# Kernel tuning notes

Hardware: AMD Instinct MI355X
Metric: run time of the kernel (lower is better)

The kernel has to match this reference:

```python
import jax, jax.numpy as jnp
import numpy as np

B, T, H, L, O = 256, 512, 512, 2, 2

def setup_inputs() -> dict:
    key = jax.random.key(0)
    ks = jax.random.split(key, 9)
    s = 0.05
    return {
        "x": jax.random.normal(ks[0], (B, T), jnp.float32),
        # input-side gate weights, layer 0 (input dim 1); gate order: [r, z, n]
        "Wi0": jax.random.normal(ks[1], (3, H, 1), jnp.float32) * s,
        "bi0": jax.random.normal(ks[2], (3, H), jnp.float32) * s,
        # input-side gate weights, layers 1..L-1 (input dim H)
        "Wi_rest": jax.random.normal(ks[3], (L - 1, 3, H, H), jnp.float32) * s,
        "bi_rest": jax.random.normal(ks[4], (L - 1, 3, H), jnp.float32) * s,
        # hidden-side gate weights for all layers
        "Wh": jax.random.normal(ks[5], (L, 3, H, H), jnp.float32) * s,
        "bh": jax.random.normal(ks[6], (L, 3, H), jnp.float32) * s,
        "fc_w": jax.random.normal(ks[7], (O, H), jnp.float32) * s,
        "fc_b": jax.random.normal(ks[8], (O,), jnp.float32) * s,
    }


def reference(x, Wi0, bi0, Wi_rest, bi_rest, Wh, bh, fc_w, fc_b):
    nL = Wh.shape[0]
    hsz = Wh.shape[-1]
    bsz = x.shape[0]

    def step(h, x_t):  # h: [L, B, H], x_t: [B]
        inp = x_t[:, None]  # [B, 1]
        new_h = []
        for l in range(nL):
            # fuse the 3 input-side and 3 hidden-side gate GEMMs into one einsum each
            if l == 0:
                gi = jnp.einsum('bi,ghi->gbh', inp, Wi0) + bi0[:, None, :]
            else:
                gi = jnp.einsum('bi,ghi->gbh', inp, Wi_rest[l - 1]) + bi_rest[l - 1, :, None, :]
            gh = jnp.einsum('bi,ghi->gbh', h[l], Wh[l]) + bh[l, :, None, :]
            r = jax.nn.sigmoid(gi[0] + gh[0])
            z = jax.nn.sigmoid(gi[1] + gh[1])
            n = jnp.tanh(gi[2] + r * gh[2])
            hl = (1.0 - z) * n + z * h[l]
            new_h.append(hl)
            inp = hl
        return jnp.stack(new_h), None

    h0 = jnp.zeros((nL, bsz, hsz), x.dtype)
    h_final, _ = jax.lax.scan(step, h0, x.T)  # scan over time axis
    return h_final[-1] @ fc_w.T + fc_b  # [B, O]
```

## Files before the change

### kernel.cpp

```cpp
#include <hip/hip_runtime.h>


#define TLEN 512
#define HDIM 512
#define MROW 32
#define NL0  8
#define WPG  24
#define GRID 192
#define U0   64
#define U1   32
#define HSZ  (MROW*HDIM)
#define ROWB 1040
#define DEPTH 4

#define RT_BAR 10000000ULL

typedef __attribute__((ext_vector_type(8))) short bf16x8;
typedef __attribute__((ext_vector_type(4))) float f32x4;

#define AT_LD64(p)   __hip_atomic_load((const unsigned long long*)(p), __ATOMIC_RELAXED, __HIP_MEMORY_SCOPE_AGENT)
#define AT_LD32(p)   __hip_atomic_load((const unsigned*)(p), __ATOMIC_RELAXED, __HIP_MEMORY_SCOPE_AGENT)
#define AT_ST16(p,v) __hip_atomic_store((unsigned short*)(p), (v), __ATOMIC_RELAXED, __HIP_MEMORY_SCOPE_AGENT)
#define AT_ST32(p,v) __hip_atomic_store((unsigned*)(p), (v), __ATOMIC_RELAXED, __HIP_MEMORY_SCOPE_AGENT)
#define AT_ST32F(p,v) __hip_atomic_store((float*)(p), (v), __ATOMIC_RELAXED, __HIP_MEMORY_SCOPE_AGENT)

__device__ __forceinline__ unsigned short f2bf(float f){
  unsigned u = __builtin_bit_cast(unsigned, f);
  u = (u + 0x7FFFu + ((u>>16)&1u)) >> 16;
  return (unsigned short)u;
}
__device__ __forceinline__ float sigm(float v){ return 1.f/(1.f + __expf(-v)); }
__device__ __forceinline__ float tanh_f(float v){ return 1.f - 2.f/(__expf(2.f*v)+1.f); }

__device__ __forceinline__ bool wait_flags(unsigned* fl, int tA, int tB, int* sab){
  if (threadIdx.x < 64){
    const int lane = threadIdx.x;
    const int tgt = (lane<8) ? tA : (lane<24 ? tB : (int)0x80000000);
    const unsigned long long t0 = __builtin_amdgcn_s_memrealtime();
    int ab = 0;
    for(;;){
      int f = (lane<24) ? (int)AT_LD32(fl + lane) : 0x7fffffff;
      if (__ballot(f >= tgt) == ~0ULL) break;
      if (__builtin_amdgcn_s_memrealtime() - t0 > RT_BAR){ ab = 1; break; }
      __builtin_amdgcn_s_sleep(1);
    }
    if (lane==0) *sab = ab;
  }
  __syncthreads();
  __builtin_amdgcn_sched_barrier(0);
  return *sab != 0;
}

__device__ __forceinline__ void stage16(const unsigned short* src, unsigned short* shDst, int tid){
  unsigned long long hb[16];
  #pragma unroll
  for (int i=0;i<16;++i)
    hb[i] = AT_LD64((const char*)src + tid*8 + i*2048);
  #pragma unroll
  for (int i=0;i<16;++i){
    int flat = tid*8 + i*2048;
    *(unsigned long long*)((char*)shDst + (flat>>10)*ROWB + (flat&1023)) = hb[i];
  }
}

extern "C" __global__ void __launch_bounds__(256,1)
gru_persistent(const float* __restrict__ x,
               const float* __restrict__ Wi0,
               const float* __restrict__ bi0,
               const float* __restrict__ Wi1,
               const float* __restrict__ bi1,
               const float* __restrict__ Wh,
               const float* __restrict__ bh,
               const float* __restrict__ fcw,
               const float* __restrict__ fcb,
               float* __restrict__ out,
               unsigned* __restrict__ flg,
               unsigned short* __restrict__ h0g,
               unsigned short* __restrict__ h1g,
               float* __restrict__ h1f)
{
  __shared__ unsigned short shA[MROW*(ROWB/2)];
  __shared__ unsigned short shB[MROW*(ROWB/2)];
  __shared__ float shG[MROW*192];
  __shared__ int s_ab;

  const int tid  = threadIdx.x;
  const int lane = tid & 63;
  const int w    = tid >> 6;
  const int grp  = blockIdx.x & 7;
  const int wgid = blockIdx.x >> 3;
  const int g32  = grp*32;

  unsigned* fl = flg + grp*64;
  unsigned short* h0 = h0g + grp*DEPTH*HSZ;
  unsigned short* h1 = h1g + grp*DEPTH*HSZ;

  if (wgid < NL0){
    const int u0   = wgid*U0;
    const int colb = w*48;

    bf16x8 bfr[3][16];
    #pragma unroll
    for (int nt=0; nt<3; ++nt){
      int col = colb + nt*16 + (lane&15);
      int g = col>>6, uu = col&63;
      const float* wrow = Wh + (size_t)(g*HDIM + u0 + uu)*HDIM;
      #pragma unroll
      for (int ks=0; ks<16; ++ks){
        int k = ks*32 + (lane>>4)*8;
        const float4 f0 = *(const float4*)(wrow + k);
        const float4 f1 = *(const float4*)(wrow + k + 4);
        bf16x8 v;
        v[0]=(short)f2bf(f0.x); v[1]=(short)f2bf(f0.y); v[2]=(short)f2bf(f0.z); v[3]=(short)f2bf(f0.w);
        v[4]=(short)f2bf(f1.x); v[5]=(short)f2bf(f1.y); v[6]=(short)f2bf(f1.z); v[7]=(short)f2bf(f1.w);
        bfr[nt][ks]=v;
      }
    }
    const int ua   = tid & 63;
    const int brow = (tid>>6)*8;
    float wi0v[3], bi0v[3], bh0v[3];
    #pragma unroll
    for (int g=0; g<3; ++g){
      wi0v[g] = Wi0[g*HDIM + u0+ua];
      bi0v[g] = bi0[g*HDIM + u0+ua];
      bh0v[g] = bh [g*HDIM + u0+ua];
    }
    float h_own[8];
    #pragma unroll
    for (int j=0;j<8;++j) h_own[j]=0.f;

    for (int s=0; s<TLEN; ++s){
      float xv[8];
      #pragma unroll
      for (int j=0;j<8;++j) xv[j] = x[(g32+brow+j)*TLEN + s];

      if (wait_flags(fl, s, s-3, &s_ab)) return;

      stage16(h0 + ((s-1)&3)*HSZ, shA, tid);
      __syncthreads();
      f32x4 acc[2][3] = {};
      #pragma unroll
      for (int ks=0; ks<16; ++ks){
        int koff = ks*64 + (lane>>4)*16;
        bf16x8 a0 = *(const bf16x8*)((const char*)shA + (lane&15)*ROWB + koff);
        bf16x8 a1 = *(const bf16x8*)((const char*)shA + ((lane&15)+16)*ROWB + koff);
        #pragma unroll
        for (int nt=0; nt<3; ++nt){
          acc[0][nt] = __builtin_amdgcn_mfma_f32_16x16x32_bf16(a0, bfr[nt][ks], acc[0][nt],0,0,0);
          acc[1][nt] = __builtin_amdgcn_mfma_f32_16x16x32_bf16(a1, bfr[nt][ks], acc[1][nt],0,0,0);
        }
      }
      #pragma unroll
      for (int mt=0; mt<2; ++mt)
        #pragma unroll
        for (int nt=0; nt<3; ++nt)
          #pragma unroll
          for (int j=0;j<4;++j){
            int b = mt*16 + (lane>>4)*4 + j;
            shG[b*192 + colb + nt*16 + (lane&15)] = acc[mt][nt][j];
          }
      __syncthreads();
      unsigned short* dstA = h0 + (s&3)*HSZ;
      #pragma unroll
      for (int j=0;j<8;++j){
        int b = brow + j;
        float G0 = shG[b*192 + ua]       + bh0v[0];
        float G1 = shG[b*192 + 64 + ua]  + bh0v[1];
        float G2 = shG[b*192 + 128 + ua] + bh0v[2];
        float r_ = sigm(fmaf(xv[j], wi0v[0], bi0v[0]) + G0);
        float z_ = sigm(fmaf(xv[j], wi0v[1], bi0v[1]) + G1);
        float n_ = tanh_f(fmaf(xv[j], wi0v[2], bi0v[2]) + r_*G2);
        float hn = (1.f - z_)*n_ + z_*h_own[j];
        h_own[j] = hn;
        AT_ST16(&dstA[b*HDIM + u0 + ua], f2bf(hn));
      }
      asm volatile("s_waitcnt vmcnt(0)" ::: "memory");
      __syncthreads();
      if (tid==0) AT_ST32(fl + wgid, (unsigned)(s+1));
    }
    if (wgid==0){
      if (wait_flags(fl, (int)0x80000000, TLEN, &s_ab)) return;
      int p = tid>>2, kl = tid&3;
      int b = p>>1, o = p&1;
      const char* h8 = (const char*)(h1f + (size_t)(g32+b)*HDIM + kl*128);
      const float2* w2 = (const float2*)(fcw + o*HDIM + kl*128);
      float a2 = 0.f;
      #pragma unroll
      for (int k=0;k<64;++k){
        unsigned long long v = AT_LD64(h8 + k*8);
        float2 hv = __builtin_bit_cast(float2, v);
        float2 wv = w2[k];
        a2 = fmaf(hv.x, wv.x, fmaf(hv.y, wv.y, a2));
      }
      a2 += __shfl_xor(a2, 1);
      a2 += __shfl_xor(a2, 2);
      if (kl==0) out[(g32+b)*2 + o] = a2 + fcb[o];
    }
  } else {
    const int u1   = (wgid-NL0)*U1;
    const int colb = (w<2) ? w*48 : 96 + (w-2)*48;

    bf16x8 bfr[3][16];
    #pragma unroll
    for (int nt=0; nt<3; ++nt){
      int col = colb + nt*16 + (lane&15);
      const float* wrow;
      if (w < 2){ int g = col>>5, uu = col&31;
        wrow = Wi1 + (size_t)(g*HDIM + u1 + uu)*HDIM;
      } else {    int c2 = col-96; int g = c2>>5, uu = c2&31;
        wrow = Wh + (size_t)((3+g)*HDIM + u1 + uu)*HDIM;
      }
      #pragma unroll
      for (int ks=0; ks<16; ++ks){
        int k = ks*32 + (lane>>4)*8;
        const float4 f0 = *(const float4*)(wrow + k);
        const float4 f1 = *(const float4*)(wrow + k + 4);
        bf16x8 v;
        v[0]=(short)f2bf(f0.x); v[1]=(short)f2bf(f0.y); v[2]=(short)f2bf(f0.z); v[3]=(short)f2bf(f0.w);
        v[4]=(short)f2bf(f1.x); v[5]=(short)f2bf(f1.y); v[6]=(short)f2bf(f1.z); v[7]=(short)f2bf(f1.w);
        bfr[nt][ks]=v;
      }
    }
    const int ua   = tid & 31;
    const int brow = (tid>>5)*4;
    float bi1v[3], bh1v[3];
    #pragma unroll
    for (int g=0; g<3; ++g){
      bi1v[g] = bi1[g*HDIM + u1+ua];
      bh1v[g] = bh [(3+g)*HDIM + u1+ua];
    }
    float h_own[4];
    #pragma unroll
    for (int j=0;j<4;++j) h_own[j]=0.f;

    for (int t=1; t<=TLEN; ++t){
      if (wait_flags(fl, t, t-1, &s_ab)) return;

      stage16(h0 + ((t-1)&3)*HSZ, shA, tid);
      stage16(h1 + ((t-2)&3)*HSZ, shB, tid);
      __syncthreads();
      const char* shSrc = (w<2) ? (const char*)shA : (const char*)shB;
      f32x4 acc[2][3] = {};
      #pragma unroll
      for (int ks=0; ks<16; ++ks){
        int koff = ks*64 + (lane>>4)*16;
        bf16x8 a0 = *(const bf16x8*)(shSrc + (lane&15)*ROWB + koff);
        bf16x8 a1 = *(const bf16x8*)(shSrc + ((lane&15)+16)*ROWB + koff);
        #pragma unroll
        for (int nt=0; nt<3; ++nt){
          acc[0][nt] = __builtin_amdgcn_mfma_f32_16x16x32_bf16(a0, bfr[nt][ks], acc[0][nt],0,0,0);
          acc[1][nt] = __builtin_amdgcn_mfma_f32_16x16x32_bf16(a1, bfr[nt][ks], acc[1][nt],0,0,0);
        }
      }
      #pragma unroll
      for (int mt=0; mt<2; ++mt)
        #pragma unroll
        for (int nt=0; nt<3; ++nt)
          #pragma unroll
          for (int j=0;j<4;++j){
            int b = mt*16 + (lane>>4)*4 + j;
            shG[b*192 + colb + nt*16 + (lane&15)] = acc[mt][nt][j];
          }
      __syncthreads();
      unsigned short* dstB = h1 + ((t-1)&3)*HSZ;
      #pragma unroll
      for (int j=0;j<4;++j){
        int b = brow + j;
        float gi0 = shG[b*192 + ua]        + bi1v[0];
        float gi1 = shG[b*192 + 32 + ua]   + bi1v[1];
        float gi2 = shG[b*192 + 64 + ua]   + bi1v[2];
        float gh0 = shG[b*192 + 96 + ua]   + bh1v[0];
        float gh1 = shG[b*192 + 128 + ua]  + bh1v[1];
        float gh2 = shG[b*192 + 160 + ua]  + bh1v[2];
        float r_ = sigm(gi0+gh0);
        float z_ = sigm(gi1+gh1);
        float n_ = tanh_f(gi2 + r_*gh2);
        float hn = (1.f - z_)*n_ + z_*h_own[j];
        h_own[j] = hn;
        AT_ST16(&dstB[b*HDIM + u1 + ua], f2bf(hn));
        if (t == TLEN) AT_ST32F(&h1f[(size_t)(g32+b)*HDIM + u1 + ua], hn);
      }
      asm volatile("s_waitcnt vmcnt(0)" ::: "memory");
      __syncthreads();
      if (tid==0) AT_ST32(fl + wgid, (unsigned)t);
    }
  }
}

extern "C" void kernel_launch(void* const* d_in, const int* in_sizes, int n_in,
                              void* d_out, int out_size, void* d_ws, size_t ws_size,
                              hipStream_t stream)
{
  const float* x   = (const float*)d_in[0];
  const float* Wi0 = (const float*)d_in[1];
  const float* bi0 = (const float*)d_in[2];
  const float* Wi1 = (const float*)d_in[3];
  const float* bi1 = (const float*)d_in[4];
  const float* Wh  = (const float*)d_in[5];
  const float* bh  = (const float*)d_in[6];
  const float* fcw = (const float*)d_in[7];
  const float* fcb = (const float*)d_in[8];
  float* out = (float*)d_out;

  unsigned*       flg = (unsigned*)d_ws;
  unsigned short* h0g = (unsigned short*)((char*)d_ws + 4096);
  unsigned short* h1g = (unsigned short*)((char*)d_ws + 4096 + 1048576);
  float*          h1f = (float*)((char*)d_ws + 4096 + 2*1048576);

  hipMemsetAsync(d_ws, 0, 4096 + 2*1048576 + 524288, stream);
  gru_persistent<<<GRID, 256, 0, stream>>>(x,Wi0,bi0,Wi1,bi1,Wh,bh,fcw,fcb,out,
                                           flg,h0g,h1g,h1f);
}
```

Before: 2.426 ms.

## Have each workgroup serve two batch groups, halving the grid to 96 blocks

Each persistent workgroup now loops over two batch groups of 32 rows per timestep instead of one, and the grid shrinks from 192 to 96 blocks. The register-resident bf16 weight fragments are reused across both groups, which halves the number of blocks that load and convert weights and that take part in flag polling. In exchange, each block runs two dependent stage/MFMA/activation/flag sequences back to back per step. That lengthens the serial critical path per timestep unless the two groups' waits overlap with each other's work.

```diff
diff --git a/kernel.cpp b/kernel.cpp
--- a/kernel.cpp
+++ b/kernel.cpp
@@ -6,7 +6,7 @@
 #define MROW 32
 #define NL0  8
 #define WPG  24
-#define GRID 192
+#define GRID 96
 #define U0   64
 #define U1   32
 #define HSZ  (MROW*HDIM)
@@ -87,13 +87,8 @@
   const int tid  = threadIdx.x;
   const int lane = tid & 63;
   const int w    = tid >> 6;
-  const int grp  = blockIdx.x & 7;
-  const int wgid = blockIdx.x >> 3;
-  const int g32  = grp*32;
-
-  unsigned* fl = flg + grp*64;
-  unsigned short* h0 = h0g + grp*DEPTH*HSZ;
-  unsigned short* h1 = h1g + grp*DEPTH*HSZ;
+  const int pair = blockIdx.x & 3;
+  const int wgid = blockIdx.x >> 2;
 
   if (wgid < NL0){
     const int u0   = wgid*U0;
@@ -125,76 +120,92 @@
       bi0v[g] = bi0[g*HDIM + u0+ua];
       bh0v[g] = bh [g*HDIM + u0+ua];
     }
-    float h_own[8];
-    #pragma unroll
-    for (int j=0;j<8;++j) h_own[j]=0.f;
+    float h_own[2][8];
+    #pragma unroll
+    for (int gi=0; gi<2; ++gi)
+      #pragma unroll
+      for (int j=0;j<8;++j) h_own[gi][j]=0.f;
 
     for (int s=0; s<TLEN; ++s){
-      float xv[8];
-      #pragma unroll
-      for (int j=0;j<8;++j) xv[j] = x[(g32+brow+j)*TLEN + s];
-
-      if (wait_flags(fl, s, s-3, &s_ab)) return;
-
-      stage16(h0 + ((s-1)&3)*HSZ, shA, tid);
-      __syncthreads();
-      f32x4 acc[2][3] = {};
-      #pragma unroll
-      for (int ks=0; ks<16; ++ks){
-        int koff = ks*64 + (lane>>4)*16;
-        bf16x8 a0 = *(const bf16x8*)((const char*)shA + (lane&15)*ROWB + koff);
-        bf16x8 a1 = *(const bf16x8*)((const char*)shA + ((lane&15)+16)*ROWB + koff);
-        #pragma unroll
-        for (int nt=0; nt<3; ++nt){
-          acc[0][nt] = __builtin_amdgcn_mfma_f32_16x16x32_bf16(a0, bfr[nt][ks], acc[0][nt],0,0,0);
-          acc[1][nt] = __builtin_amdgcn_mfma_f32_16x16x32_bf16(a1, bfr[nt][ks], acc[1][nt],0,0,0);
-        }
-      }
-      #pragma unroll
-      for (int mt=0; mt<2; ++mt)
-        #pragma unroll
-        for (int nt=0; nt<3; ++nt)
+      #pragma unroll
+      for (int gi=0; gi<2; ++gi){
+        const int grp = pair*2 + gi;
+        const int g32 = grp*32;
+        unsigned* fl = flg + grp*64;
+        unsigned short* h0 = h0g + grp*DEPTH*HSZ;
+
+        float xv[8];
+        #pragma unroll
+        for (int j=0;j<8;++j) xv[j] = x[(g32+brow+j)*TLEN + s];
+
+        if (wait_flags(fl, s, s-3, &s_ab)) return;
+
+        stage16(h0 + ((s-1)&3)*HSZ, shA, tid);
+        __syncthreads();
+        f32x4 acc[2][3] = {};
+        #pragma unroll
+        for (int ks=0; ks<16; ++ks){
+          int koff = ks*64 + (lane>>4)*16;
+          bf16x8 a0 = *(const bf16x8*)((const char*)shA + (lane&15)*ROWB + koff);
+          bf16x8 a1 = *(const bf16x8*)((const char*)shA + ((lane&15)+16)*ROWB + koff);
           #pragma unroll
-          for (int j=0;j<4;++j){
-            int b = mt*16 + (lane>>4)*4 + j;
-            shG[b*192 + colb + nt*16 + (lane&15)] = acc[mt][nt][j];
+          for (int nt=0; nt<3; ++nt){
+            acc[0][nt] = __builtin_amdgcn_mfma_f32_16x16x32_bf16(a0, bfr[nt][ks], acc[0][nt],0,0,0);
+            acc[1][nt] = __builtin_amdgcn_mfma_f32_16x16x32_bf16(a1, bfr[nt][ks], acc[1][nt],0,0,0);
           }
-      __syncthreads();
-      unsigned short* dstA = h0 + (s&3)*HSZ;
-      #pragma unroll
-      for (int j=0;j<8;++j){
-        int b = brow + j;
-        float G0 = shG[b*192 + ua]       + bh0v[0];
-        float G1 = shG[b*192 + 64 + ua]  + bh0v[1];
-        float G2 = shG[b*192 + 128 + ua] + bh0v[2];
-        float r_ = sigm(fmaf(xv[j], wi0v[0], bi0v[0]) + G0);
-        float z_ = sigm(fmaf(xv[j], wi0v[1], bi0v[1]) + G1);
-        float n_ = tanh_f(fmaf(xv[j], wi0v[2], bi0v[2]) + r_*G2);
-        float hn = (1.f - z_)*n_ + z_*h_own[j];
-        h_own[j] = hn;
-        AT_ST16(&dstA[b*HDIM + u0 + ua], f2bf(hn));
-      }
-      asm volatile("s_waitcnt vmcnt(0)" ::: "memory");
-      __syncthreads();
-      if (tid==0) AT_ST32(fl + wgid, (unsigned)(s+1));
+        }
+        #pragma unroll
+        for (int mt=0; mt<2; ++mt)
+          #pragma unroll
+          for (int nt=0; nt<3; ++nt)
+            #pragma unroll
+            for (int j=0;j<4;++j){
+              int b = mt*16 + (lane>>4)*4 + j;
+              shG[b*192 + colb + nt*16 + (lane&15)] = acc[mt][nt][j];
+            }
+        __syncthreads();
+        unsigned short* dstA = h0 + (s&3)*HSZ;
+        #pragma unroll
+        for (int j=0;j<8;++j){
+          int b = brow + j;
+          float G0 = shG[b*192 + ua]       + bh0v[0];
+          float G1 = shG[b*192 + 64 + ua]  + bh0v[1];
+          float G2 = shG[b*192 + 128 + ua] + bh0v[2];
+          float r_ = sigm(fmaf(xv[j], wi0v[0], bi0v[0]) + G0);
+          float z_ = sigm(fmaf(xv[j], wi0v[1], bi0v[1]) + G1);
+          float n_ = tanh_f(fmaf(xv[j], wi0v[2], bi0v[2]) + r_*G2);
+          float hn = (1.f - z_)*n_ + z_*h_own[gi][j];
+          h_own[gi][j] = hn;
+          AT_ST16(&dstA[b*HDIM + u0 + ua], f2bf(hn));
+        }
+        asm volatile("s_waitcnt vmcnt(0)" ::: "memory");
+        __syncthreads();
+        if (tid==0) AT_ST32(fl + wgid, (unsigned)(s+1));
+      }
     }
     if (wgid==0){
-      if (wait_flags(fl, (int)0x80000000, TLEN, &s_ab)) return;
-      int p = tid>>2, kl = tid&3;
-      int b = p>>1, o = p&1;
-      const char* h8 = (const char*)(h1f + (size_t)(g32+b)*HDIM + kl*128);
-      const float2* w2 = (const float2*)(fcw + o*HDIM + kl*128);
-      float a2 = 0.f;
-      #pragma unroll
-      for (int k=0;k<64;++k){
-        unsigned long long v = AT_LD64(h8 + k*8);
-        float2 hv = __builtin_bit_cast(float2, v);
-        float2 wv = w2[k];
-        a2 = fmaf(hv.x, wv.x, fmaf(hv.y, wv.y, a2));
-      }
-      a2 += __shfl_xor(a2, 1);
-      a2 += __shfl_xor(a2, 2);
-      if (kl==0) out[(g32+b)*2 + o] = a2 + fcb[o];
+      #pragma unroll
+      for (int gi=0; gi<2; ++gi){
+        const int grp = pair*2 + gi;
+        const int g32 = grp*32;
+        unsigned* fl = flg + grp*64;
+        if (wait_flags(fl, (int)0x80000000, TLEN, &s_ab)) return;
+        int p = tid>>2, kl = tid&3;
+        int b = p>>1, o = p&1;
+        const char* h8 = (const char*)(h1f + (size_t)(g32+b)*HDIM + kl*128);
+        const float2* w2 = (const float2*)(fcw + o*HDIM + kl*128);
+        float a2 = 0.f;
+        #pragma unroll
+        for (int k=0;k<64;++k){
+          unsigned long long v = AT_LD64(h8 + k*8);
+          float2 hv = __builtin_bit_cast(float2, v);
+          float2 wv = w2[k];
+          a2 = fmaf(hv.x, wv.x, fmaf(hv.y, wv.y, a2));
+        }
+        a2 += __shfl_xor(a2, 1);
+        a2 += __shfl_xor(a2, 2);
+        if (kl==0) out[(g32+b)*2 + o] = a2 + fcb[o];
+      }
     }
   } else {
     const int u1   = (wgid-NL0)*U1;
@@ -229,60 +240,71 @@
       bi1v[g] = bi1[g*HDIM + u1+ua];
       bh1v[g] = bh [(3+g)*HDIM + u1+ua];
     }
-    float h_own[4];
-    #pragma unroll
-    for (int j=0;j<4;++j) h_own[j]=0.f;
+    float h_own[2][4];
+    #pragma unroll
+    for (int gi=0; gi<2; ++gi)
+      #pragma unroll
+      for (int j=0;j<4;++j) h_own[gi][j]=0.f;
 
     for (int t=1; t<=TLEN; ++t){
-      if (wait_flags(fl, t, t-1, &s_ab)) return;
-
-      stage16(h0 + ((t-1)&3)*HSZ, shA, tid);
-      stage16(h1 + ((t-2)&3)*HSZ, shB, tid);
-      __syncthreads();
-      const char* shSrc = (w<2) ? (const char*)shA : (const char*)shB;
-      f32x4 acc[2][3] = {};
-      #pragma unroll
-      for (int ks=0; ks<16; ++ks){
-        int koff = ks*64 + (lane>>4)*16;
-        bf16x8 a0 = *(const bf16x8*)(shSrc + (lane&15)*ROWB + koff);
-        bf16x8 a1 = *(const bf16x8*)(shSrc + ((lane&15)+16)*ROWB + koff);
-        #pragma unroll
-        for (int nt=0; nt<3; ++nt){
-          acc[0][nt] = __builtin_amdgcn_mfma_f32_16x16x32_bf16(a0, bfr[nt][ks], acc[0][nt],0,0,0);
-          acc[1][nt] = __builtin_amdgcn_mfma_f32_16x16x32_bf16(a1, bfr[nt][ks], acc[1][nt],0,0,0);
-        }
-      }
-      #pragma unroll
-      for (int mt=0; mt<2; ++mt)
-        #pragma unroll
-        for (int nt=0; nt<3; ++nt)
+      #pragma unroll
+      for (int gi=0; gi<2; ++gi){
+        const int grp = pair*2 + gi;
+        const int g32 = grp*32;
+        unsigned* fl = flg + grp*64;
+        unsigned short* h0 = h0g + grp*DEPTH*HSZ;
+        unsigned short* h1 = h1g + grp*DEPTH*HSZ;
+
+        if (wait_flags(fl, t, t-1, &s_ab)) return;
+
+        stage16(h0 + ((t-1)&3)*HSZ, shA, tid);
+        stage16(h1 + ((t-2)&3)*HSZ, shB, tid);
+        __syncthreads();
+        const char* shSrc = (w<2) ? (const char*)shA : (const char*)shB;
+        f32x4 acc[2][3] = {};
+        #pragma unroll
+        for (int ks=0; ks<16; ++ks){
+          int koff = ks*64 + (lane>>4)*16;
+          bf16x8 a0 = *(const bf16x8*)(shSrc + (lane&15)*ROWB + koff);
+          bf16x8 a1 = *(const bf16x8*)(shSrc + ((lane&15)+16)*ROWB + koff);
           #pragma unroll
-          for (int j=0;j<4;++j){
-            int b = mt*16 + (lane>>4)*4 + j;
-            shG[b*192 + colb + nt*16 + (lane&15)] = acc[mt][nt][j];
+          for (int nt=0; nt<3; ++nt){
+            acc[0][nt] = __builtin_amdgcn_mfma_f32_16x16x32_bf16(a0, bfr[nt][ks], acc[0][nt],0,0,0);
+            acc[1][nt] = __builtin_amdgcn_mfma_f32_16x16x32_bf16(a1, bfr[nt][ks], acc[1][nt],0,0,0);
           }
-      __syncthreads();
-      unsigned short* dstB = h1 + ((t-1)&3)*HSZ;
-      #pragma unroll
-      for (int j=0;j<4;++j){
-        int b = brow + j;
-        float gi0 = shG[b*192 + ua]        + bi1v[0];
-        float gi1 = shG[b*192 + 32 + ua]   + bi1v[1];
-        float gi2 = shG[b*192 + 64 + ua]   + bi1v[2];
-        float gh0 = shG[b*192 + 96 + ua]   + bh1v[0];
-        float gh1 = shG[b*192 + 128 + ua]  + bh1v[1];
-        float gh2 = shG[b*192 + 160 + ua]  + bh1v[2];
-        float r_ = sigm(gi0+gh0);
-        float z_ = sigm(gi1+gh1);
-        float n_ = tanh_f(gi2 + r_*gh2);
-        float hn = (1.f - z_)*n_ + z_*h_own[j];
-        h_own[j] = hn;
-        AT_ST16(&dstB[b*HDIM + u1 + ua], f2bf(hn));
-        if (t == TLEN) AT_ST32F(&h1f[(size_t)(g32+b)*HDIM + u1 + ua], hn);
-      }
-      asm volatile("s_waitcnt vmcnt(0)" ::: "memory");
-      __syncthreads();
-      if (tid==0) AT_ST32(fl + wgid, (unsigned)t);
+        }
+        #pragma unroll
+        for (int mt=0; mt<2; ++mt)
+          #pragma unroll
+          for (int nt=0; nt<3; ++nt)
+            #pragma unroll
+            for (int j=0;j<4;++j){
+              int b = mt*16 + (lane>>4)*4 + j;
+              shG[b*192 + colb + nt*16 + (lane&15)] = acc[mt][nt][j];
+            }
+        __syncthreads();
+        unsigned short* dstB = h1 + ((t-1)&3)*HSZ;
+        #pragma unroll
+        for (int j=0;j<4;++j){
+          int b = brow + j;
+          float gi0 = shG[b*192 + ua]        + bi1v[0];
+          float gi1 = shG[b*192 + 32 + ua]   + bi1v[1];
+          float gi2 = shG[b*192 + 64 + ua]   + bi1v[2];
+          float gh0 = shG[b*192 + 96 + ua]   + bh1v[0];
+          float gh1 = shG[b*192 + 128 + ua]  + bh1v[1];
+          float gh2 = shG[b*192 + 160 + ua]  + bh1v[2];
+          float r_ = sigm(gi0+gh0);
+          float z_ = sigm(gi1+gh1);
+          float n_ = tanh_f(gi2 + r_*gh2);
+          float hn = (1.f - z_)*n_ + z_*h_own[gi][j];
+          h_own[gi][j] = hn;
+          AT_ST16(&dstB[b*HDIM + u1 + ua], f2bf(hn));
+          if (t == TLEN) AT_ST32F(&h1f[(size_t)(g32+b)*HDIM + u1 + ua], hn);
+        }
+        asm volatile("s_waitcnt vmcnt(0)" ::: "memory");
+        __syncthreads();
+        if (tid==0) AT_ST32(fl + wgid, (unsigned)t);
+      }
     }
   }
 }
```

Result: slower. 4.542 ms (+87.2%).

## Pad sync flags to separate cache lines and split layer-1 waits per source

Applied to the files above, without the earlier changes.

Each workgroup's progress flag now sits at a 64-byte stride instead of being packed together, so polling and flag stores should no longer share cache lines. The workspace offset and memset size grow to hold the larger flag area. The layer-1 workers now wait first on the layer-1 flags and start loading the previous h1 state, then wait on the layer-0 flags before loading h0, overlapping one global load with the other wait. Sigmoid and tanh use the hardware reciprocal intrinsic instead of a full division, at some cost in precision.

```diff
diff --git a/kernel.cpp b/kernel.cpp
--- a/kernel.cpp
+++ b/kernel.cpp
@@ -29,8 +29,8 @@
   u = (u + 0x7FFFu + ((u>>16)&1u)) >> 16;
   return (unsigned short)u;
 }
-__device__ __forceinline__ float sigm(float v){ return 1.f/(1.f + __expf(-v)); }
-__device__ __forceinline__ float tanh_f(float v){ return 1.f - 2.f/(__expf(2.f*v)+1.f); }
+__device__ __forceinline__ float sigm(float v){ return __builtin_amdgcn_rcpf(1.f + __expf(-v)); }
+__device__ __forceinline__ float tanh_f(float v){ return 1.f - 2.f*__builtin_amdgcn_rcpf(__expf(2.f*v)+1.f); }
 
 __device__ __forceinline__ bool wait_flags(unsigned* fl, int tA, int tB, int* sab){
   if (threadIdx.x < 64){
@@ -39,7 +39,7 @@
     const unsigned long long t0 = __builtin_amdgcn_s_memrealtime();
     int ab = 0;
     for(;;){
-      int f = (lane<24) ? (int)AT_LD32(fl + lane) : 0x7fffffff;
+      int f = (lane<24) ? (int)AT_LD32(fl + lane*16) : 0x7fffffff;
       if (__ballot(f >= tgt) == ~0ULL) break;
       if (__builtin_amdgcn_s_memrealtime() - t0 > RT_BAR){ ab = 1; break; }
       __builtin_amdgcn_s_sleep(1);
@@ -91,7 +91,7 @@
   const int wgid = blockIdx.x >> 3;
   const int g32  = grp*32;
 
-  unsigned* fl = flg + grp*64;
+  unsigned* fl = flg + grp*512;
   unsigned short* h0 = h0g + grp*DEPTH*HSZ;
   unsigned short* h1 = h1g + grp*DEPTH*HSZ;
 
@@ -176,7 +176,7 @@
       }
       asm volatile("s_waitcnt vmcnt(0)" ::: "memory");
       __syncthreads();
-      if (tid==0) AT_ST32(fl + wgid, (unsigned)(s+1));
+      if (tid==0) AT_ST32(fl + wgid*16, (unsigned)(s+1));
     }
     if (wgid==0){
       if (wait_flags(fl, (int)0x80000000, TLEN, &s_ab)) return;
@@ -234,10 +234,27 @@
     for (int j=0;j<4;++j) h_own[j]=0.f;
 
     for (int t=1; t<=TLEN; ++t){
-      if (wait_flags(fl, t, t-1, &s_ab)) return;
-
-      stage16(h0 + ((t-1)&3)*HSZ, shA, tid);
-      stage16(h1 + ((t-2)&3)*HSZ, shB, tid);
+      const unsigned short* srcA = h0 + ((t-1)&3)*HSZ;
+      const unsigned short* srcB = h1 + ((t-2)&3)*HSZ;
+
+      if (wait_flags(fl, (int)0x80000000, t-1, &s_ab)) return;
+      unsigned long long hb1[16];
+      #pragma unroll
+      for (int i=0;i<16;++i)
+        hb1[i] = AT_LD64((const char*)srcB + tid*8 + i*2048);
+
+      if (wait_flags(fl, t, (int)0x80000000, &s_ab)) return;
+      unsigned long long hb0[16];
+      #pragma unroll
+      for (int i=0;i<16;++i)
+        hb0[i] = AT_LD64((const char*)srcA + tid*8 + i*2048);
+
+      #pragma unroll
+      for (int i=0;i<16;++i){
+        int flat = tid*8 + i*2048;
+        *(unsigned long long*)((char*)shA + (flat>>10)*ROWB + (flat&1023)) = hb0[i];
+        *(unsigned long long*)((char*)shB + (flat>>10)*ROWB + (flat&1023)) = hb1[i];
+      }
       __syncthreads();
       const char* shSrc = (w<2) ? (const char*)shA : (const char*)shB;
       f32x4 acc[2][3] = {};
@@ -282,7 +299,7 @@
       }
       asm volatile("s_waitcnt vmcnt(0)" ::: "memory");
       __syncthreads();
-      if (tid==0) AT_ST32(fl + wgid, (unsigned)t);
+      if (tid==0) AT_ST32(fl + wgid*16, (unsigned)t);
     }
   }
 }
@@ -303,11 +320,11 @@
   float* out = (float*)d_out;
 
   unsigned*       flg = (unsigned*)d_ws;
-  unsigned short* h0g = (unsigned short*)((char*)d_ws + 4096);
-  unsigned short* h1g = (unsigned short*)((char*)d_ws + 4096 + 1048576);
-  float*          h1f = (float*)((char*)d_ws + 4096 + 2*1048576);
-
-  hipMemsetAsync(d_ws, 0, 4096 + 2*1048576 + 524288, stream);
+  unsigned short* h0g = (unsigned short*)((char*)d_ws + 16384);
+  unsigned short* h1g = (unsigned short*)((char*)d_ws + 16384 + 1048576);
+  float*          h1f = (float*)((char*)d_ws + 16384 + 2*1048576);
+
+  hipMemsetAsync(d_ws, 0, 16384 + 2*1048576 + 524288, stream);
   gru_persistent<<<GRID, 256, 0, stream>>>(x,Wi0,bi0,Wi1,bi1,Wh,bh,fcw,fcb,out,
                                            flg,h0g,h1g,h1f);
 }
```

After: 2.420 ms. About the same (-0.2%).

## Replace per-step flag barriers with epoch-tagged hidden-state words polled directly

Applied to the files above, without the earlier changes.

Each bf16 hidden value is now stored as a 32-bit word carrying its timestep epoch in the upper half. Consumers poll the staged data until every epoch matches, which replaces most per-step flag waits and the vmcnt drain plus syncthreads before each flag store. Layer-0 workgroups drop the shared-memory gate round trip and apply the gate math directly from MFMA accumulators. Reciprocal intrinsics are used in the sigmoid and tanh. The cost is double the global traffic for hidden-state exchange and repeated spinning reloads of whole slabs, and flags are now only needed for ring-buffer back-pressure.

```diff
diff --git a/kernel.cpp b/kernel.cpp
--- a/kernel.cpp
+++ b/kernel.cpp
@@ -5,11 +5,10 @@
 #define HDIM 512
 #define MROW 32
 #define NL0  8
-#define WPG  24
 #define GRID 192
 #define U0   64
 #define U1   32
-#define HSZ  (MROW*HDIM)
+#define SLOTD (MROW*HDIM)
 #define ROWB 1040
 #define DEPTH 4
 
@@ -20,7 +19,6 @@
 
 #define AT_LD64(p)   __hip_atomic_load((const unsigned long long*)(p), __ATOMIC_RELAXED, __HIP_MEMORY_SCOPE_AGENT)
 #define AT_LD32(p)   __hip_atomic_load((const unsigned*)(p), __ATOMIC_RELAXED, __HIP_MEMORY_SCOPE_AGENT)
-#define AT_ST16(p,v) __hip_atomic_store((unsigned short*)(p), (v), __ATOMIC_RELAXED, __HIP_MEMORY_SCOPE_AGENT)
 #define AT_ST32(p,v) __hip_atomic_store((unsigned*)(p), (v), __ATOMIC_RELAXED, __HIP_MEMORY_SCOPE_AGENT)
 #define AT_ST32F(p,v) __hip_atomic_store((float*)(p), (v), __ATOMIC_RELAXED, __HIP_MEMORY_SCOPE_AGENT)
 
@@ -29,17 +27,17 @@
   u = (u + 0x7FFFu + ((u>>16)&1u)) >> 16;
   return (unsigned short)u;
 }
-__device__ __forceinline__ float sigm(float v){ return 1.f/(1.f + __expf(-v)); }
-__device__ __forceinline__ float tanh_f(float v){ return 1.f - 2.f/(__expf(2.f*v)+1.f); }
-
-__device__ __forceinline__ bool wait_flags(unsigned* fl, int tA, int tB, int* sab){
+__device__ __forceinline__ float sigm(float v){ return __builtin_amdgcn_rcpf(1.f + __expf(-v)); }
+__device__ __forceinline__ float tanh_f(float v){ return 1.f - 2.f*__builtin_amdgcn_rcpf(__expf(2.f*v)+1.f); }
+
+__device__ __forceinline__ bool wait_f1(unsigned* fl, int tB, int* sab){
   if (threadIdx.x < 64){
     const int lane = threadIdx.x;
-    const int tgt = (lane<8) ? tA : (lane<24 ? tB : (int)0x80000000);
+    const int tgt = (lane<16) ? tB : (int)0x80000000;
     const unsigned long long t0 = __builtin_amdgcn_s_memrealtime();
     int ab = 0;
     for(;;){
-      int f = (lane<24) ? (int)AT_LD32(fl + lane) : 0x7fffffff;
+      int f = (lane<16) ? (int)AT_LD32(fl + lane*16) : 0x7fffffff;
       if (__ballot(f >= tgt) == ~0ULL) break;
       if (__builtin_amdgcn_s_memrealtime() - t0 > RT_BAR){ ab = 1; break; }
       __builtin_amdgcn_s_sleep(1);
@@ -51,16 +49,34 @@
   return *sab != 0;
 }
 
-__device__ __forceinline__ void stage16(const unsigned short* src, unsigned short* shDst, int tid){
-  unsigned long long hb[16];
+__device__ __forceinline__ void stageV(const unsigned* src, unsigned short* shDst,
+                                       int tid, unsigned ep, int* sab){
+  const unsigned long long epat =
+      ((unsigned long long)ep << 16) | ((unsigned long long)ep << 48);
+  const unsigned long long emask = 0xFFFF0000FFFF0000ULL;
+  unsigned long long hb[32];
+  const unsigned long long t0 = __builtin_amdgcn_s_memrealtime();
+  for(;;){
+    #pragma unroll
+    for (int i=0;i<32;++i)
+      hb[i] = AT_LD64((const char*)src + tid*8 + i*2048);
+    unsigned long long bad = 0;
+    #pragma unroll
+    for (int i=0;i<32;++i) bad |= (hb[i] ^ epat) & emask;
+    if (!bad) break;
+    if (__builtin_amdgcn_s_memrealtime() - t0 > RT_BAR){ *sab = 1; break; }
+  }
   #pragma unroll
-  for (int i=0;i<16;++i)
-    hb[i] = AT_LD64((const char*)src + tid*8 + i*2048);
+  for (int i=0;i<32;++i){
+    unsigned v = (unsigned)(hb[i] & 0xFFFFu) | ((unsigned)((hb[i]>>32)&0xFFFFu) << 16);
+    *(unsigned*)((char*)shDst + i*ROWB + tid*4) = v;
+  }
+}
+
+__device__ __forceinline__ void zeroSh(unsigned short* shDst, int tid){
   #pragma unroll
-  for (int i=0;i<16;++i){
-    int flat = tid*8 + i*2048;
-    *(unsigned long long*)((char*)shDst + (flat>>10)*ROWB + (flat&1023)) = hb[i];
-  }
+  for (int i=0;i<32;++i)
+    *(unsigned*)((char*)shDst + i*ROWB + tid*4) = 0u;
 }
 
 extern "C" __global__ void __launch_bounds__(256,1)
@@ -75,8 +91,8 @@
                const float* __restrict__ fcb,
                float* __restrict__ out,
                unsigned* __restrict__ flg,
-               unsigned short* __restrict__ h0g,
-               unsigned short* __restrict__ h1g,
+               unsigned* __restrict__ h0g,
+               unsigned* __restrict__ h1g,
                float* __restrict__ h1f)
 {
   __shared__ unsigned short shA[MROW*(ROWB/2)];
@@ -91,20 +107,21 @@
   const int wgid = blockIdx.x >> 3;
   const int g32  = grp*32;
 
-  unsigned* fl = flg + grp*64;
-  unsigned short* h0 = h0g + grp*DEPTH*HSZ;
-  unsigned short* h1 = h1g + grp*DEPTH*HSZ;
+  if (tid==0) s_ab = 0;
+  __syncthreads();
+
+  unsigned* fl = flg + grp*256;
+  unsigned* h0 = h0g + grp*DEPTH*SLOTD;
+  unsigned* h1 = h1g + grp*DEPTH*SLOTD;
 
   if (wgid < NL0){
-    const int u0   = wgid*U0;
-    const int colb = w*48;
+    const int u0  = wgid*U0;
+    const int ua2 = w*16 + (lane&15);
 
     bf16x8 bfr[3][16];
     #pragma unroll
     for (int nt=0; nt<3; ++nt){
-      int col = colb + nt*16 + (lane&15);
-      int g = col>>6, uu = col&63;
-      const float* wrow = Wh + (size_t)(g*HDIM + u0 + uu)*HDIM;
+      const float* wrow = Wh + (size_t)(nt*HDIM + u0 + ua2)*HDIM;
       #pragma unroll
       for (int ks=0; ks<16; ++ks){
         int k = ks*32 + (lane>>4)*8;
@@ -116,28 +133,32 @@
         bfr[nt][ks]=v;
       }
     }
-    const int ua   = tid & 63;
-    const int brow = (tid>>6)*8;
     float wi0v[3], bi0v[3], bh0v[3];
     #pragma unroll
     for (int g=0; g<3; ++g){
-      wi0v[g] = Wi0[g*HDIM + u0+ua];
-      bi0v[g] = bi0[g*HDIM + u0+ua];
-      bh0v[g] = bh [g*HDIM + u0+ua];
+      wi0v[g] = Wi0[g*HDIM + u0+ua2];
+      bi0v[g] = bi0[g*HDIM + u0+ua2];
+      bh0v[g] = bh [g*HDIM + u0+ua2];
     }
     float h_own[8];
     #pragma unroll
     for (int j=0;j<8;++j) h_own[j]=0.f;
 
     for (int s=0; s<TLEN; ++s){
-      float xv[8];
-      #pragma unroll
-      for (int j=0;j<8;++j) xv[j] = x[(g32+brow+j)*TLEN + s];
-
-      if (wait_flags(fl, s, s-3, &s_ab)) return;
-
-      stage16(h0 + ((s-1)&3)*HSZ, shA, tid);
+      float xv[2][4];
+      #pragma unroll
+      for (int mt=0; mt<2; ++mt)
+        #pragma unroll
+        for (int j=0;j<4;++j)
+          xv[mt][j] = x[(g32 + mt*16 + (lane>>4)*4 + j)*TLEN + s];
+
+      if (wait_f1(fl, s-3, &s_ab)) return;
+
+      if (s==0) zeroSh(shA, tid);
+      else      stageV(h0 + ((s-1)&3)*SLOTD, shA, tid, (unsigned)s, &s_ab);
       __syncthreads();
+      if (s_ab) return;
+
       f32x4 acc[2][3] = {};
       #pragma unroll
       for (int ks=0; ks<16; ++ks){
@@ -150,36 +171,27 @@
           acc[1][nt] = __builtin_amdgcn_mfma_f32_16x16x32_bf16(a1, bfr[nt][ks], acc[1][nt],0,0,0);
         }
       }
+      unsigned* dst32 = h0 + (s&3)*SLOTD;
+      const unsigned epw = (unsigned)(s+1) << 16;
       #pragma unroll
       for (int mt=0; mt<2; ++mt)
         #pragma unroll
-        for (int nt=0; nt<3; ++nt)
-          #pragma unroll
-          for (int j=0;j<4;++j){
-            int b = mt*16 + (lane>>4)*4 + j;
-            shG[b*192 + colb + nt*16 + (lane&15)] = acc[mt][nt][j];
-          }
-      __syncthreads();
-      unsigned short* dstA = h0 + (s&3)*HSZ;
-      #pragma unroll
-      for (int j=0;j<8;++j){
-        int b = brow + j;
-        float G0 = shG[b*192 + ua]       + bh0v[0];
-        float G1 = shG[b*192 + 64 + ua]  + bh0v[1];
-        float G2 = shG[b*192 + 128 + ua] + bh0v[2];
-        float r_ = sigm(fmaf(xv[j], wi0v[0], bi0v[0]) + G0);
-        float z_ = sigm(fmaf(xv[j], wi0v[1], bi0v[1]) + G1);
-        float n_ = tanh_f(fmaf(xv[j], wi0v[2], bi0v[2]) + r_*G2);
-        float hn = (1.f - z_)*n_ + z_*h_own[j];
-        h_own[j] = hn;
-        AT_ST16(&dstA[b*HDIM + u0 + ua], f2bf(hn));
-      }
-      asm volatile("s_waitcnt vmcnt(0)" ::: "memory");
-      __syncthreads();
-      if (tid==0) AT_ST32(fl + wgid, (unsigned)(s+1));
+        for (int j=0;j<4;++j){
+          int b = mt*16 + (lane>>4)*4 + j;
+          float G0 = acc[mt][0][j] + bh0v[0];
+          float G1 = acc[mt][1][j] + bh0v[1];
+          float G2 = acc[mt][2][j] + bh0v[2];
+          float xvv = xv[mt][j];
+          float r_ = sigm(fmaf(xvv, wi0v[0], bi0v[0]) + G0);
+          float z_ = sigm(fmaf(xvv, wi0v[1], bi0v[1]) + G1);
+          float n_ = tanh_f(fmaf(xvv, wi0v[2], bi0v[2]) + r_*G2);
+          float hn = (1.f - z_)*n_ + z_*h_own[mt*4+j];
+          h_own[mt*4+j] = hn;
+          AT_ST32(dst32 + b*HDIM + u0 + ua2, epw | (unsigned)f2bf(hn));
+        }
     }
     if (wgid==0){
-      if (wait_flags(fl, (int)0x80000000, TLEN, &s_ab)) return;
+      if (wait_f1(fl, TLEN, &s_ab)) return;
       int p = tid>>2, kl = tid&3;
       int b = p>>1, o = p&1;
       const char* h8 = (const char*)(h1f + (size_t)(g32+b)*HDIM + kl*128);
@@ -197,7 +209,8 @@
       if (kl==0) out[(g32+b)*2 + o] = a2 + fcb[o];
     }
   } else {
-    const int u1   = (wgid-NL0)*U1;
+    const int wg1  = wgid - NL0;
+    const int u1   = wg1*U1;
     const int colb = (w<2) ? w*48 : 96 + (w-2)*48;
 
     bf16x8 bfr[3][16];
@@ -234,11 +247,13 @@
     for (int j=0;j<4;++j) h_own[j]=0.f;
 
     for (int t=1; t<=TLEN; ++t){
-      if (wait_flags(fl, t, t-1, &s_ab)) return;
-
-      stage16(h0 + ((t-1)&3)*HSZ, shA, tid);
-      stage16(h1 + ((t-2)&3)*HSZ, shB, tid);
+      stageV(h0 + ((t-1)&3)*SLOTD, shA, tid, (unsigned)t, &s_ab);
+      if (t==1) zeroSh(shB, tid);
+      else      stageV(h1 + ((t-2)&3)*SLOTD, shB, tid, (unsigned)(t-1), &s_ab);
       __syncthreads();
+      if (s_ab) return;
+      if (tid==0 && t<TLEN) AT_ST32(fl + wg1*16, (unsigned)t);
+
       const char* shSrc = (w<2) ? (const char*)shA : (const char*)shB;
       f32x4 acc[2][3] = {};
       #pragma unroll
@@ -262,7 +277,8 @@
             shG[b*192 + colb + nt*16 + (lane&15)] = acc[mt][nt][j];
           }
       __syncthreads();
-      unsigned short* dstB = h1 + ((t-1)&3)*HSZ;
+      unsigned* dst32 = h1 + ((t-1)&3)*SLOTD;
+      const unsigned epw = (unsigned)t << 16;
       #pragma unroll
       for (int j=0;j<4;++j){
         int b = brow + j;
@@ -277,13 +293,13 @@
         float n_ = tanh_f(gi2 + r_*gh2);
         float hn = (1.f - z_)*n_ + z_*h_own[j];
         h_own[j] = hn;
-        AT_ST16(&dstB[b*HDIM + u1 + ua], f2bf(hn));
+        AT_ST32(dst32 + b*HDIM + u1 + ua, epw | (unsigned)f2bf(hn));
         if (t == TLEN) AT_ST32F(&h1f[(size_t)(g32+b)*HDIM + u1 + ua], hn);
       }
-      asm volatile("s_waitcnt vmcnt(0)" ::: "memory");
-      __syncthreads();
-      if (tid==0) AT_ST32(fl + wgid, (unsigned)t);
-    }
+    }
+    asm volatile("s_waitcnt vmcnt(0)" ::: "memory");
+    __syncthreads();
+    if (tid==0) AT_ST32(fl + wg1*16, (unsigned)TLEN);
   }
 }
 
@@ -302,12 +318,12 @@
   const float* fcb = (const float*)d_in[8];
   float* out = (float*)d_out;
 
-  unsigned*       flg = (unsigned*)d_ws;
-  unsigned short* h0g = (unsigned short*)((char*)d_ws + 4096);
-  unsigned short* h1g = (unsigned short*)((char*)d_ws + 4096 + 1048576);
-  float*          h1f = (float*)((char*)d_ws + 4096 + 2*1048576);
-
-  hipMemsetAsync(d_ws, 0, 4096 + 2*1048576 + 524288, stream);
+  unsigned* flg = (unsigned*)d_ws;
+  unsigned* h0g = (unsigned*)((char*)d_ws + 16384);
+  unsigned* h1g = (unsigned*)((char*)d_ws + 16384 + 2097152);
+  float*    h1f = (float*)((char*)d_ws + 16384 + 2*2097152);
+
+  hipMemsetAsync(d_ws, 0, 16384 + 2*2097152 + 524288, stream);
   gru_persistent<<<GRID, 256, 0, stream>>>(x,Wi0,bi0,Wi1,bi1,Wh,bh,fcw,fcb,out,
                                            flg,h0g,h1g,h1f);
 }
```

Result: no change. 2.386 ms (-1.6%).
